# Optimization experiments

Hardware: AMD Instinct MI355X
Metric: run time of the kernel (lower is better)

## Reference

```python
import jax, jax.numpy as jnp
import numpy as np


def _pdist2squared(x, y):
    # x: [B, 3, N], y: [B, 3, M] -> squared pairwise dists [B, N, M]
    xx = jnp.sum(x * x, axis=1)[:, :, None]          # [B, N, 1]
    yy = jnp.sum(y * y, axis=1)[:, None, :]          # [B, 1, M]
    dist = xx + yy - 2.0 * jnp.einsum('bdn,bdm->bnm', x, y)
    dist = jnp.where(jnp.isnan(dist), 0.0, dist)     # dist[dist != dist] = 0
    return jnp.maximum(dist, 0.0)                    # clamp to [0, inf)


def setup_inputs() -> dict:
    key = jax.random.key(0)
    k1, k2, k3 = jax.random.split(key, 3)
    B, N, M, C = 4, 16384, 4096, 64
    return {
        'points': jax.random.normal(k1, (B, 3, N), dtype=jnp.float32),
        'new_points': jax.random.normal(k2, (B, 3, M), dtype=jnp.float32),
        'features': jax.random.normal(k3, (B, C, N), dtype=jnp.float32),
        'num_samples': 32,
    }


def reference(points, new_points, features, num_samples):
    # kNN indices: smallest num_samples dists along N for each query m
    dist = _pdist2squared(points, new_points)            # [B, N, M]
    neg = -jnp.transpose(dist, (0, 2, 1))                # [B, M, N]
    _, idx = jax.lax.top_k(neg, num_samples)             # [B, M, K]

    # group_gather_by_index: gather along last axis by idx -> [B, C, M, K]
    def gather(t):
        return jnp.take_along_axis(t[:, :, None, :], idx[:, None, :, :], axis=3)

    grouped_points = gather(points) - new_points[:, :, :, None]   # [B, 3, M, K]
    grouped_features = gather(features)                            # [B, C, M, K]
    return jnp.concatenate([grouped_points, grouped_features], axis=1)
```

## Files before the change

kernel.cpp:

```cpp
#include <hip/hip_runtime.h>

static constexpr int Bn = 4;
static constexpr int Nn = 16384;
static constexpr int Mn = 4096;
static constexpr int Cn = 64;
static constexpr int Kn = 32;

static constexpr int CHUNK   = 2048;
static constexpr int WPB     = 8;
static constexpr int THREADS = WPB * 64;
static constexpr int NCHUNK  = Nn / CHUNK;
static constexpr int NGROUP  = CHUNK / 256;

static constexpr float EPS = 4e-3f;

typedef unsigned long long ull;

__device__ __forceinline__ ull bcast64(ull v, int srclane) {
  unsigned lo = (unsigned)__builtin_amdgcn_readlane((int)(unsigned)v, srclane);
  unsigned hi = (unsigned)__builtin_amdgcn_readlane((int)(v >> 32), srclane);
  return ((ull)hi << 32) | lo;
}

__device__ __forceinline__ int lanes_below(ull m) {
  return (int)__builtin_amdgcn_mbcnt_hi((unsigned)(m >> 32),
            __builtin_amdgcn_mbcnt_lo((unsigned)m, 0u));
}

__device__ __forceinline__ ull permute_push64(int dstlane, ull v) {
  const int idx = dstlane << 2;
  int lo = __builtin_amdgcn_ds_permute(idx, (int)(unsigned)v);
  int hi = __builtin_amdgcn_ds_permute(idx, (int)(v >> 32));
  return ((ull)(unsigned)hi << 32) | (unsigned)lo;
}

__device__ __forceinline__ ull sort64_asc(ull key, int lane) {
#pragma unroll
  for (int k = 2; k <= 64; k <<= 1) {
#pragma unroll
    for (int j = k >> 1; j > 0; j >>= 1) {
      const ull other = __shfl_xor(key, j);
      const bool keep_min = ((lane & j) == 0) == ((lane & k) == 0);
      const bool take = keep_min ? (other < key) : (other > key);
      key = take ? other : key;
    }
  }
  return key;
}

__device__ __forceinline__ ull merge_top32(ull lst, ull batch, int lane) {
  const ull bl = __shfl_xor(batch, 31);
  ull L = (bl < lst) ? bl : lst;
#pragma unroll
  for (int j = 16; j > 0; j >>= 1) {
    const ull other = __shfl_xor(L, j);
    const bool keep_min = (lane & j) == 0;
    const bool take = keep_min ? (other < L) : (other > L);
    L = take ? other : L;
  }
  return (lane < 32) ? L : ~0ull;
}

__device__ __forceinline__ void set_tauf(ull tau, float yyq, float& tau_f) {
  const unsigned th = (unsigned)(tau >> 32);
  tau_f = (th == 0xFFFFFFFFu) ? -__builtin_inff()
                              : (yyq - __uint_as_float(th) - EPS) * 0.5f;
}

__device__ __forceinline__ void flush_pend(ull& pend, int& pcnt, ull& lst,
                                           ull& tau, float& tau_f,
                                           float yyq, int lane) {
  const ull key = sort64_asc(pend, lane);
  lst = merge_top32(lst, key, lane);
  tau = bcast64(lst, 31);
  set_tauf(tau, yyq, tau_f);
  pend = ~0ull;
  pcnt = 0;
}

__global__ __launch_bounds__(256) void transpose_f(
    const float* __restrict__ F, float* __restrict__ FT) {
  __shared__ float t[64][65];
  const int tid = threadIdx.x;
  const int bid = blockIdx.x;
  const int xcd = bid & 7;
  const int b   = xcd >> 1;
  const int nt  = (bid >> 3) * 2 + (xcd & 1);
  const float* Fb = F + (size_t)b * Cn * Nn;
  float* FTb = FT + (size_t)b * Nn * Cn;
  for (int sub = 0; sub < 4; ++sub) {
    const int nbase = nt * 256 + sub * 64;
#pragma unroll
    for (int i = 0; i < 16; ++i) {
      const int c = (tid >> 6) + 4 * i;
      t[c][tid & 63] = Fb[(size_t)c * Nn + nbase + (tid & 63)];
    }
    __syncthreads();
#pragma unroll
    for (int i = 0; i < 16; ++i) {
      const int nn = (tid >> 6) + 4 * i;
      FTb[(size_t)(nbase + nn) * Cn + (tid & 63)] = t[tid & 63][nn];
    }
    __syncthreads();
  }
}

__global__ __launch_bounds__(THREADS, 8) void knn_group(
    const float* __restrict__ P,
    const float* __restrict__ Q,
    const float* __restrict__ FT,
    float* __restrict__ out)
{
#pragma clang fp contract(off)
  __shared__ float lds[4][CHUNK];

  const int tid  = threadIdx.x;
  const int lane = tid & 63;
  const int wid  = tid >> 6;
  const int bid  = blockIdx.x;
  const int xcd  = bid & 7;
  const int b    = xcd >> 1;
  const int tile = (bid >> 3) * 2 + (xcd & 1);
  const int m    = tile * WPB + wid;

  const float* Pb = P + (size_t)b * 3 * Nn;
  const float* Qb = Q + (size_t)b * 3 * Mn;

  const float qx = Qb[m];
  const float qy = Qb[Mn + m];
  const float qz = Qb[2 * Mn + m];
  const float yyq = (qx * qx + qy * qy) + qz * qz;

  const int t4 = tid * 4;

  {
    float4 vx = *(const float4*)(Pb + t4);
    float4 vy = *(const float4*)(Pb + Nn + t4);
    float4 vz = *(const float4*)(Pb + 2 * Nn + t4);
    float4 vh;
    vh.x = -0.5f * ((vx.x * vx.x + vy.x * vy.x) + vz.x * vz.x);
    vh.y = -0.5f * ((vx.y * vx.y + vy.y * vy.y) + vz.y * vz.y);
    vh.z = -0.5f * ((vx.z * vx.z + vy.z * vy.z) + vz.z * vz.z);
    vh.w = -0.5f * ((vx.w * vx.w + vy.w * vy.w) + vz.w * vz.w);
    *(float4*)&lds[0][t4] = vx;
    *(float4*)&lds[1][t4] = vy;
    *(float4*)&lds[2][t4] = vz;
    *(float4*)&lds[3][t4] = vh;
  }
  __syncthreads();

  ull lst  = ~0ull;
  ull tau  = ~0ull;
  ull pend = ~0ull;
  int pcnt = 0;
  float tau_f;
  set_tauf(tau, yyq, tau_f);

  for (int ch = 0; ch < NCHUNK; ++ch) {
    const int n0 = ch * CHUNK;

    float4 nx, ny, nz;
    if (ch + 1 < NCHUNK) {
      nx = *(const float4*)(Pb + (n0 + CHUNK) + t4);
      ny = *(const float4*)(Pb + Nn + (n0 + CHUNK) + t4);
      nz = *(const float4*)(Pb + 2 * Nn + (n0 + CHUNK) + t4);
    }

#pragma unroll
    for (int g = 0; g < NGROUP; ++g) {
      const int p = g * 256 + lane * 4;
      const float4 rx = *(const float4*)&lds[0][p];
      const float4 ry = *(const float4*)&lds[1][p];
      const float4 rz = *(const float4*)&lds[2][p];
      const float4 rh = *(const float4*)&lds[3][p];

      const float s0 = fmaf(rz.x, qz, fmaf(ry.x, qy, fmaf(rx.x, qx, rh.x)));
      const float s1 = fmaf(rz.y, qz, fmaf(ry.y, qy, fmaf(rx.y, qx, rh.y)));
      const float s2 = fmaf(rz.z, qz, fmaf(ry.z, qy, fmaf(rx.z, qx, rh.z)));
      const float s3 = fmaf(rz.w, qz, fmaf(ry.w, qy, fmaf(rx.w, qx, rh.w)));

      const float smax = fmaxf(fmaxf(s0, s1), fmaxf(s2, s3));
      if (__any(smax >= tau_f)) {
        const unsigned nb = (unsigned)(n0 + p);
#define SUBW(SX, CX, CY, CZ, CH_, NOFF)                                       \
        {                                                                     \
          ull mj = __ballot((SX) >= tau_f);                                   \
          if (mj) {                                                           \
            const float xxv = -2.0f * (CH_);                                  \
            const float ddv = fmaf((CZ), qz, fmaf((CY), qy, (CX) * qx));      \
            const float dv  = fmaxf((xxv + yyq) - 2.0f * ddv, 0.0f);          \
            const ull kj = ((ull)__float_as_uint(dv) << 32) | (unsigned)(NOFF);\
            int c = (int)__popcll(mj);                                        \
            if (pcnt + c > 63) {                                              \
              flush_pend(pend, pcnt, lst, tau, tau_f, yyq, lane);             \
              mj = __ballot((SX) >= tau_f);                                   \
              c  = (int)__popcll(mj);                                         \
            }                                                                 \
            if (c > 63) {                  \
              const ull key = sort64_asc(kj, lane);                           \
              lst = merge_top32(lst, key, lane);                              \
              tau = bcast64(lst, 31);                                         \
              set_tauf(tau, yyq, tau_f);                                      \
            } else if (c) {                                                   \
              const int prefix = lanes_below(mj);                             \
              const bool pass = (mj >> lane) & 1ull;                          \
              const int dst = pass ? (pcnt + prefix) : 63;                    \
              const ull got = permute_push64(dst, kj);                        \
              const bool take = (lane >= pcnt) && (lane < pcnt + c);          \
              pend = take ? got : pend;                                       \
              pcnt += c;                                                      \
            }                                                                 \
          }                                                                   \
        }
        SUBW(s0, rx.x, ry.x, rz.x, rh.x, nb + 0u)
        SUBW(s1, rx.y, ry.y, rz.y, rh.y, nb + 1u)
        SUBW(s2, rx.z, ry.z, rz.z, rh.z, nb + 2u)
        SUBW(s3, rx.w, ry.w, rz.w, rh.w, nb + 3u)
#undef SUBW
      }
    }
    __syncthreads();

    if (ch + 1 < NCHUNK) {
      float4 vh;
      vh.x = -0.5f * ((nx.x * nx.x + ny.x * ny.x) + nz.x * nz.x);
      vh.y = -0.5f * ((nx.y * nx.y + ny.y * ny.y) + nz.y * nz.y);
      vh.z = -0.5f * ((nx.z * nx.z + ny.z * ny.z) + nz.z * nz.z);
      vh.w = -0.5f * ((nx.w * nx.w + ny.w * ny.w) + nz.w * nz.w);
      *(float4*)&lds[0][t4] = nx;
      *(float4*)&lds[1][t4] = ny;
      *(float4*)&lds[2][t4] = nz;
      *(float4*)&lds[3][t4] = vh;
      __syncthreads();
    }
  }

  if (pcnt > 0) flush_pend(pend, pcnt, lst, tau, tau_f, yyq, lane);

  const size_t MK = (size_t)Mn * Kn;
  float* outb = out + (size_t)b * (3 + Cn) * MK;

  if (lane < 32) {
    const int idx = (int)(__shfl(lst, lane) & 0xffffffffull);
    const float px = Pb[idx];
    const float py = Pb[Nn + idx];
    const float pz = Pb[2 * Nn + idx];
    outb[0 * MK + (size_t)m * Kn + lane] = px - qx;
    outb[1 * MK + (size_t)m * Kn + lane] = py - qy;
    outb[2 * MK + (size_t)m * Kn + lane] = pz - qz;
  }

  const float* FTb = FT + (size_t)b * Nn * Cn;
  const int r = lane & 15;
  const int q = lane >> 4;
#pragma unroll
  for (int p2 = 0; p2 < 2; ++p2) {
    const int k = p2 * 16 + r;
    const int idxk = (int)(__shfl(lst, k) & 0xffffffffull);
    const float* row = FTb + (size_t)idxk * Cn;
    float4 v[4];
#pragma unroll
    for (int i = 0; i < 4; ++i)
      v[i] = *(const float4*)(row + (q + 4 * i) * 4);
#pragma unroll
    for (int i = 0; i < 4; ++i) {
      const int c = (q + 4 * i) * 4;
      float* o = outb + (size_t)(3 + c) * MK + (size_t)m * Kn + k;
      o[0 * MK] = v[i].x;
      o[1 * MK] = v[i].y;
      o[2 * MK] = v[i].z;
      o[3 * MK] = v[i].w;
    }
  }
}

extern "C" void kernel_launch(void* const* d_in, const int* in_sizes, int n_in,
                              void* d_out, int out_size, void* d_ws, size_t ws_size,
                              hipStream_t stream) {
  (void)in_sizes; (void)n_in; (void)out_size; (void)ws_size;
  const float* P = (const float*)d_in[0];
  const float* Q = (const float*)d_in[1];
  const float* F = (const float*)d_in[2];
  float* out = (float*)d_out;
  float* FT  = (float*)d_ws;

  hipLaunchKernelGGL(transpose_f, dim3(256), dim3(256), 0, stream, F, FT);
  hipLaunchKernelGGL(knn_group, dim3(Bn * Mn / WPB), dim3(THREADS), 0, stream,
                     P, Q, FT, out);
}
```

Measured before the change: 226.7 us.

## Load point chunks directly into LDS via global_load_lds and relax launch bounds

Replaces the register-staged prefetch of the next point chunk with direct global-to-LDS loads at the start of each chunk, then computes the -0.5*|p|^2 term from LDS after a barrier. Launch bounds minimum blocks drop from 8 to 4, allowing more registers per thread. This removes VGPR pressure from the prefetch registers but loses the overlap of the next chunk's load with current compute and adds barriers per chunk.

```diff
diff --git a/kernel.cpp b/kernel.cpp
--- a/kernel.cpp
+++ b/kernel.cpp
@@ -32,6 +32,12 @@
   int lo = __builtin_amdgcn_ds_permute(idx, (int)(unsigned)v);
   int hi = __builtin_amdgcn_ds_permute(idx, (int)(v >> 32));
   return ((ull)(unsigned)hi << 32) | (unsigned)lo;
+}
+
+__device__ __forceinline__ void gl_lds16(const float* g, float* l) {
+  __builtin_amdgcn_global_load_lds(
+      (const __attribute__((address_space(1))) void*)g,
+      (__attribute__((address_space(3))) void*)l, 16, 0, 0);
 }
 
 __device__ __forceinline__ ull sort64_asc(ull key, int lane) {
@@ -105,7 +111,7 @@
   }
 }
 
-__global__ __launch_bounds__(THREADS, 8) void knn_group(
+__global__ __launch_bounds__(THREADS, 4) void knn_group(
     const float* __restrict__ P,
     const float* __restrict__ Q,
     const float* __restrict__ FT,
@@ -133,22 +139,6 @@
 
   const int t4 = tid * 4;
 
-  {
-    float4 vx = *(const float4*)(Pb + t4);
-    float4 vy = *(const float4*)(Pb + Nn + t4);
-    float4 vz = *(const float4*)(Pb + 2 * Nn + t4);
-    float4 vh;
-    vh.x = -0.5f * ((vx.x * vx.x + vy.x * vy.x) + vz.x * vz.x);
-    vh.y = -0.5f * ((vx.y * vx.y + vy.y * vy.y) + vz.y * vz.y);
-    vh.z = -0.5f * ((vx.z * vx.z + vy.z * vy.z) + vz.z * vz.z);
-    vh.w = -0.5f * ((vx.w * vx.w + vy.w * vy.w) + vz.w * vz.w);
-    *(float4*)&lds[0][t4] = vx;
-    *(float4*)&lds[1][t4] = vy;
-    *(float4*)&lds[2][t4] = vz;
-    *(float4*)&lds[3][t4] = vh;
-  }
-  __syncthreads();
-
   ull lst  = ~0ull;
   ull tau  = ~0ull;
   ull pend = ~0ull;
@@ -159,12 +149,27 @@
   for (int ch = 0; ch < NCHUNK; ++ch) {
     const int n0 = ch * CHUNK;
 
-    float4 nx, ny, nz;
-    if (ch + 1 < NCHUNK) {
-      nx = *(const float4*)(Pb + (n0 + CHUNK) + t4);
-      ny = *(const float4*)(Pb + Nn + (n0 + CHUNK) + t4);
-      nz = *(const float4*)(Pb + 2 * Nn + (n0 + CHUNK) + t4);
-    }
+    {
+      const int base = wid * 256;
+      const float* g0 = Pb + n0 + base + lane * 4;
+      gl_lds16(g0,          &lds[0][base]);
+      gl_lds16(g0 + Nn,     &lds[1][base]);
+      gl_lds16(g0 + 2 * Nn, &lds[2][base]);
+    }
+    __syncthreads();
+
+    {
+      const float4 vx = *(const float4*)&lds[0][t4];
+      const float4 vy = *(const float4*)&lds[1][t4];
+      const float4 vz = *(const float4*)&lds[2][t4];
+      float4 vh;
+      vh.x = -0.5f * ((vx.x * vx.x + vy.x * vy.x) + vz.x * vz.x);
+      vh.y = -0.5f * ((vx.y * vx.y + vy.y * vy.y) + vz.y * vz.y);
+      vh.z = -0.5f * ((vx.z * vx.z + vy.z * vy.z) + vz.z * vz.z);
+      vh.w = -0.5f * ((vx.w * vx.w + vy.w * vy.w) + vz.w * vz.w);
+      *(float4*)&lds[3][t4] = vh;
+    }
+    __syncthreads();
 
 #pragma unroll
     for (int g = 0; g < NGROUP; ++g) {
@@ -220,19 +225,6 @@
       }
     }
     __syncthreads();
-
-    if (ch + 1 < NCHUNK) {
-      float4 vh;
-      vh.x = -0.5f * ((nx.x * nx.x + ny.x * ny.x) + nz.x * nz.x);
-      vh.y = -0.5f * ((nx.y * nx.y + ny.y * ny.y) + nz.y * nz.y);
-      vh.z = -0.5f * ((nx.z * nx.z + ny.z * ny.z) + nz.z * nz.z);
-      vh.w = -0.5f * ((nx.w * nx.w + ny.w * ny.w) + nz.w * nz.w);
-      *(float4*)&lds[0][t4] = nx;
-      *(float4*)&lds[1][t4] = ny;
-      *(float4*)&lds[2][t4] = nz;
-      *(float4*)&lds[3][t4] = vh;
-      __syncthreads();
-    }
   }
 
   if (pcnt > 0) flush_pend(pend, pcnt, lst, tau, tau_f, yyq, lane);
```

Result: slower. 235.5 us (+3.9%).
